# Performance work log

Hardware: AMD Instinct MI355X
Metric: run time of the kernel (lower is better)

Reference implementation:

```python
import jax, jax.numpy as jnp
import numpy as np

N = 50000      # nodes
E = 250000     # edges
IN = 256       # in_channels
OUT = 256      # out_channels
H = 4          # heads
C = OUT // H   # per-head channels = 64
MSG = 128
TIME = 64
ED = MSG + TIME + 2   # edge_dim = 194


def _glorot(k, shape):
    return (jax.random.normal(k, shape, jnp.float32) / np.sqrt(shape[0])).astype(jnp.float32)


def setup_inputs() -> dict:
    ks = jax.random.split(jax.random.key(0), 16)
    z = lambda: jnp.zeros((H * C,), jnp.float32)
    inp = {
        "x": jax.random.normal(ks[0], (N, IN), jnp.float32),
        "edge_index": jax.random.randint(ks[1], (2, E), 0, N),
        "edge_attr": jax.random.normal(ks[2], (E, ED), jnp.float32),
        # conv1 params (in_channels=IN)
        "Wq1": _glorot(ks[3], (IN, H * C)), "bq1": z(),
        "Wk1": _glorot(ks[4], (IN, H * C)), "bk1": z(),
        "Wv1": _glorot(ks[5], (IN, H * C)), "bv1": z(),
        "We1": _glorot(ks[6], (ED, H * C)),              # lin_edge has no bias in PyG
        "Ws1": _glorot(ks[7], (IN, H * C)), "bs1": z(),  # skip/root connection
        # conv2 params (in_channels=OUT)
        "Wq2": _glorot(ks[8], (OUT, H * C)), "bq2": z(),
        "Wk2": _glorot(ks[9], (OUT, H * C)), "bk2": z(),
        "Wv2": _glorot(ks[10], (OUT, H * C)), "bv2": z(),
        "We2": _glorot(ks[11], (ED, H * C)),
        "Ws2": _glorot(ks[12], (OUT, H * C)), "bs2": z(),
    }
    return inp


def _tconv(x, src, dst, edge_attr, Wq, bq, Wk, bk, Wv, bv, We, Ws, bs):
    """PyG TransformerConv (heads=H, concat=True, root_weight=True), eval mode."""
    n = x.shape[0]
    q = (x @ Wq + bq).reshape(n, H, C)
    k = (x @ Wk + bk).reshape(n, H, C)
    v = (x @ Wv + bv).reshape(n, H, C)
    e = (edge_attr @ We).reshape(-1, H, C)          # [E,H,C]
    kj = k[src] + e                                  # key + edge embedding
    vj = v[src] + e                                  # value + edge embedding
    logits = jnp.einsum('ehc,ehc->eh', q[dst], kj) / np.sqrt(C)  # [E,H]
    # segment softmax over incoming edges of each dst node
    m = jax.lax.stop_gradient(jax.ops.segment_max(logits, dst, num_segments=n))
    ex = jnp.exp(logits - m[dst])
    denom = jax.ops.segment_sum(ex, dst, num_segments=n)
    a = ex / (denom[dst] + 1e-16)                    # [E,H]
    agg = jax.ops.segment_sum(vj * a[:, :, None], dst, num_segments=n)  # [N,H,C]
    return agg.reshape(n, H * C) + x @ Ws + bs


def reference(x, edge_index, edge_attr,
              Wq1, bq1, Wk1, bk1, Wv1, bv1, We1, Ws1, bs1,
              Wq2, bq2, Wk2, bk2, Wv2, bv2, We2, Ws2, bs2):
    src, dst = edge_index[0], edge_index[1]
    h = jax.nn.relu(_tconv(x, src, dst, edge_attr,
                           Wq1, bq1, Wk1, bk1, Wv1, bv1, We1, Ws1, bs1))
    # dropout is identity in eval mode
    return _tconv(h, src, dst, edge_attr,
                  Wq2, bq2, Wk2, bk2, Wv2, bv2, We2, Ws2, bs2)
```

## Files before the change

kernel.cpp:

```cpp
#include <hip/hip_runtime.h>

#define N_NODES 50000
#define N_EDGES 250000
#define DIM 256
#define ED 194
#define EDP 224
#define MP_NODE 50048
#define MP_EDGE 250112

typedef __bf16 bf16x8 __attribute__((ext_vector_type(8)));
typedef float f32x4 __attribute__((ext_vector_type(4)));
typedef short s16x8 __attribute__((ext_vector_type(8)));
typedef short s16x4 __attribute__((ext_vector_type(4)));
typedef unsigned short u16x8 __attribute__((ext_vector_type(8)));

__device__ __forceinline__ float bf2f(unsigned short b){
  union { unsigned int u; float f; } v; v.u = ((unsigned int)b)<<16; return v.f;
}
__device__ __forceinline__ short f2bf(float f){
  union { float f; unsigned int u; } v; v.f = f;
  unsigned int u = v.u;
  return (short)((u + 0x7fffu + ((u>>16)&1u))>>16);
}

__device__ __forceinline__ void gload_lds16(const void* g, void* l){
  __builtin_amdgcn_global_load_lds(
      (const __attribute__((address_space(1))) unsigned int*)g,
      (__attribute__((address_space(3))) unsigned int*)l, 16, 0, 0);
}

__global__ __launch_bounds__(256) void convert_x_kernel(
    const float* __restrict__ x, short* __restrict__ xb, int* __restrict__ deg)
{
  int idx = blockIdx.x*256 + threadIdx.x;
  if (idx < N_NODES) deg[idx] = 0;
  s16x4 o;
  if (idx < N_NODES*64){
    float4 a = *(const float4*)(x + (size_t)idx*4);
    o[0]=f2bf(a.x); o[1]=f2bf(a.y); o[2]=f2bf(a.z); o[3]=f2bf(a.w);
  } else {
    o[0]=0; o[1]=0; o[2]=0; o[3]=0;
  }
  *(s16x4*)(xb + (size_t)idx*4) = o;
}

#define E_ROWS 32
__global__ __launch_bounds__(256) void convert_e_kernel(
    const float* __restrict__ ea, short* __restrict__ eb)
{
  __shared__ float lds[E_ROWS*ED];
  int row0 = blockIdx.x * E_ROWS;
  int tid = threadIdx.x;
  int base = row0 * ED;
  int valid = N_EDGES*ED - base;

  for (int i = tid; i < E_ROWS*ED/4; i += 256){
    float4 v;
    if (i*4 < valid) v = *(const float4*)(ea + base + i*4);
    else             v = make_float4(0.f,0.f,0.f,0.f);
    *(float4*)(lds + i*4) = v;
  }
  __syncthreads();

  for (int u = tid; u < E_ROWS*28; u += 256){
    int row = u / 28;
    int c8  = u - row*28;
    int col = c8*8;
    s16x8 o;
    if (col + 8 <= ED){
      #pragma unroll
      for (int j2=0;j2<4;j2++){
        float2 f = *(const float2*)(lds + row*ED + col + j2*2);
        o[j2*2]   = f2bf(f.x);
        o[j2*2+1] = f2bf(f.y);
      }
    } else {
      #pragma unroll
      for (int j=0;j<8;j++){
        int c = col + j;
        o[j] = (c < ED) ? f2bf(lds[row*ED + c]) : (short)0;
      }
    }
    *(s16x8*)(eb + (size_t)(row0+row)*EDP + col) = o;
  }
}

__global__ __launch_bounds__(256) void prep_weights(
    const float* __restrict__ Wq, const float* __restrict__ Wk,
    const float* __restrict__ Wv, const float* __restrict__ Ws,
    const float* __restrict__ We,
    const float* __restrict__ b0, const float* __restrict__ b1,
    const float* __restrict__ b2, const float* __restrict__ b3,
    short* __restrict__ WtN, short* __restrict__ WtE, float* __restrict__ biasN)
{
  __shared__ short lds[64*65];
  int b = blockIdx.x, tid = threadIdx.x;
  if (b < 64){
    int mat = b>>4, tile = b&15;
    int i0 = (tile>>2)*64, o0 = (tile&3)*64;
    const float* W = (mat==0)?Wq:((mat==1)?Wk:((mat==2)?Wv:Ws));
    #pragma unroll
    for (int t=0;t<16;t++){
      int idx = t*256+tid; int r = idx>>6, c = idx&63;
      lds[r*65+c] = f2bf(W[(size_t)(i0+r)*256 + o0 + c]);
    }
    __syncthreads();
    #pragma unroll
    for (int t=0;t<4;t++){
      int idx = t*256+tid; int r = idx>>4, c4 = (idx&15)*4;
      s16x4 o;
      o[0]=lds[(c4+0)*65+r]; o[1]=lds[(c4+1)*65+r];
      o[2]=lds[(c4+2)*65+r]; o[3]=lds[(c4+3)*65+r];
      *(s16x4*)(WtN + (mat<<16) + (o0+r)*256 + i0 + c4) = o;
    }
  } else if (b < 80){
    int b2 = b-64;
    int k0 = (b2>>2)*64, o0 = (b2&3)*64;
    #pragma unroll
    for (int t=0;t<16;t++){
      int idx = t*256+tid; int r = idx>>6, c = idx&63;
      int k = k0+r;
      lds[r*65+c] = (k<ED) ? f2bf(We[(size_t)k*256 + o0 + c]) : (short)0;
    }
    __syncthreads();
    #pragma unroll
    for (int t=0;t<4;t++){
      int idx = t*256+tid; int r = idx>>4, c4 = (idx&15)*4;
      if (k0 + c4 < EDP){
        s16x4 o;
        o[0]=lds[(c4+0)*65+r]; o[1]=lds[(c4+1)*65+r];
        o[2]=lds[(c4+2)*65+r]; o[3]=lds[(c4+3)*65+r];
        *(s16x4*)(WtE + (o0+r)*EDP + k0 + c4) = o;
      }
    }
  } else {
    for (int t = tid; t < 1024; t += 256){
      const float* bb = (t<256)?b0:((t<512)?b1:((t<768)?b2:b3));
      biasN[t] = bb[t&255];
    }
  }
}

__global__ __launch_bounds__(256) void count_deg(const int* __restrict__ dst, int* __restrict__ deg){
  int e = blockIdx.x*256 + threadIdx.x;
  if (e < N_EDGES) atomicAdd(&deg[dst[e]], 1);
}
#define SCAN_NBLK 196
__global__ __launch_bounds__(256) void scan_p1(const int* __restrict__ deg, int* __restrict__ part){
  int t = threadIdx.x;
  int i = blockIdx.x*256 + t;
  int v = (i<N_NODES)? deg[i] : 0;
  #pragma unroll
  for (int off=32; off; off>>=1) v += __shfl_xor(v, off, 64);
  __shared__ int s[4];
  if ((t&63)==0) s[t>>6] = v;
  __syncthreads();
  if (t==0) part[blockIdx.x] = s[0]+s[1]+s[2]+s[3];
}
__global__ __launch_bounds__(256) void scan_p2(int* __restrict__ part){
  __shared__ int s[256];
  int t = threadIdx.x;
  int v = (t<SCAN_NBLK)? part[t] : 0;
  s[t] = v; __syncthreads();
  for (int off=1; off<256; off<<=1){
    int x = (t>=off)? s[t-off] : 0;
    __syncthreads();
    s[t] += x;
    __syncthreads();
  }
  part[t] = (t==0)? 0 : s[t-1];
}
__global__ __launch_bounds__(256) void scan_p3(const int* __restrict__ deg,
    const int* __restrict__ part, int* __restrict__ rowptr, int* __restrict__ cursor){
  __shared__ int s[256];
  int t = threadIdx.x;
  int i = blockIdx.x*256 + t;
  int v = (i<N_NODES)? deg[i] : 0;
  s[t] = v; __syncthreads();
  for (int off=1; off<256; off<<=1){
    int x = (t>=off)? s[t-off] : 0;
    __syncthreads();
    s[t] += x;
    __syncthreads();
  }
  if (i < N_NODES){ rowptr[i+1] = part[blockIdx.x] + s[t]; cursor[i] = 0; }
  if (i == 0) rowptr[0] = 0;
}
__global__ __launch_bounds__(256) void scatter_edges(
    const int* __restrict__ src, const int* __restrict__ dst,
    const int* __restrict__ rowptr, int* __restrict__ cursor, int2* __restrict__ csr)
{
  int e = blockIdx.x*256 + threadIdx.x;
  if (e < N_EDGES){
    int d = dst[e];
    int pos = atomicAdd(&cursor[d], 1);
    csr[rowptr[d] + pos] = make_int2(src[e]<<11, e<<9);
  }
}

template<int K, int NLD, bool HAS_BIAS>
__global__ __launch_bounds__(256) void gemm_bt(
    const short* __restrict__ A, const short* __restrict__ Bt,
    const float* __restrict__ bias, short* __restrict__ out, int M)
{
  __shared__ short As[128*32];
  __shared__ short Bs[128*32];
  int tid = threadIdx.x;
  int lane = tid & 63, wave = tid >> 6;
  int m0 = blockIdx.x*128, n0 = blockIdx.y*128;

  int srow = wave*16 + (lane&15);
  int scol = (lane>>4)*8;
  const short* gA = A + (size_t)(m0+srow)*K + scol;
  const short* gB = Bt + (size_t)(n0+srow)*K + scol;
  short* ldsA1 = As + wave*512;
  short* ldsA2 = As + 2048 + wave*512;
  short* ldsB1 = Bs + wave*512;
  short* ldsB2 = Bs + 2048 + wave*512;

  int wr = wave>>1, wc = wave&1;
  int fr = lane & 15;
  int kq = lane >> 4;
  f32x4 acc[4][4];
  #pragma unroll
  for (int a=0;a<4;a++)
    #pragma unroll
    for (int b=0;b<4;b++) acc[a][b] = (f32x4){0.f,0.f,0.f,0.f};

  const short* ar = As + wr*2048 + kq*128 + fr*8;
  const short* br = Bs + wc*2048 + kq*128 + fr*8;

  for (int k0=0; k0<K; k0+=32){
    __syncthreads();
    gload_lds16(gA + k0,                ldsA1);
    gload_lds16(gA + (size_t)64*K + k0, ldsA2);
    gload_lds16(gB + k0,                ldsB1);
    gload_lds16(gB + (size_t)64*K + k0, ldsB2);
    __syncthreads();

    bf16x8 af[4], bf[4];
    #pragma unroll
    for (int fm=0;fm<4;fm++) af[fm] = *(const bf16x8*)(ar + fm*512);
    #pragma unroll
    for (int fn=0;fn<4;fn++) bf[fn] = *(const bf16x8*)(br + fn*512);
    #pragma unroll
    for (int fm=0;fm<4;fm++)
      #pragma unroll
      for (int fn=0;fn<4;fn++)
        acc[fm][fn] = __builtin_amdgcn_mfma_f32_16x16x32_bf16(af[fm], bf[fn], acc[fm][fn], 0, 0, 0);
  }

  int cr = (lane>>4)*4;
  int cc = lane & 15;
  #pragma unroll
  for (int fm=0;fm<4;fm++){
    #pragma unroll
    for (int fn=0;fn<4;fn++){
      int col = n0 + wc*64 + fn*16 + cc;
      float bv = HAS_BIAS ? bias[col] : 0.f;
      #pragma unroll
      for (int i=0;i<4;i++){
        int row = m0 + wr*64 + fm*16 + cr + i;
        if (row < M) out[(size_t)row*NLD + col] = f2bf(acc[fm][fn][i] + bv);
      }
    }
  }
}

__global__ __launch_bounds__(256) void edge_phase_kernel(
    const short* __restrict__ QKVS, const short* __restrict__ Eemb,
    const int* __restrict__ rowptr, const int2* __restrict__ csr,
    short* __restrict__ out_bf, float* __restrict__ out_f, int relu)
{
  int tid = threadIdx.x, wave = tid>>6, lane = tid&63;
  int node = blockIdx.x*4 + wave;
  if (node >= N_NODES){
    if (node < MP_NODE && out_bf){
      s16x4 z; z[0]=0; z[1]=0; z[2]=0; z[3]=0;
      *(s16x4*)(out_bf + (size_t)node*256 + lane*4) = z;
    }
    return;
  }
  int half = lane>>5;
  int hl   = lane&31;
  int c8   = hl*8;
  const unsigned short* base = (const unsigned short*)QKVS + (size_t)node*1024;

  u16x8 qu = *(const u16x8*)(base + c8);
  float q[8];
  #pragma unroll
  for (int j=0;j<8;j++) q[j] = bf2f(qu[j])*0.125f;

  int beg = rowptr[node], end = rowptr[node+1];
  float l = 0.f;
  float a[8];
  #pragma unroll
  for (int j=0;j<8;j++) a[j] = 0.f;
  int kb = 512 + hl*16;
  int ebo = hl*16;

  for (int idx = beg; idx < end; idx += 2){
    int j = idx + half;
    int jc = (j < end) ? j : (end-1);
    int2 se = csr[jc];
    const char* Kp = (const char*)QKVS + (unsigned)(se.x + kb);
    const char* Ep = (const char*)Eemb + (unsigned)(se.y + ebo);
    u16x8 ku = *(const u16x8*)Kp;
    u16x8 vu = *(const u16x8*)(Kp + 512);
    u16x8 eu = *(const u16x8*)Ep;
    float vv[8];
    float t = 0.f;
    #pragma unroll
    for (int c=0;c<8;c++){
      float ef = bf2f(eu[c]);
      float kf = bf2f(ku[c]) + ef;
      vv[c]    = bf2f(vu[c]) + ef;
      t += q[c]*kf;
    }
    t += __shfl_xor(t, 1, 64);
    t += __shfl_xor(t, 2, 64);
    t += __shfl_xor(t, 4, 64);
    float p = (j < end) ? __expf(t) : 0.f;
    l += p;
    #pragma unroll
    for (int c=0;c<8;c++) a[c] += p*vv[c];
  }

  l += __shfl_xor(l, 32, 64);
  #pragma unroll
  for (int c=0;c<8;c++) a[c] += __shfl_xor(a[c], 32, 64);

  float inv = (l > 0.f) ? 1.0f/l : 0.f;
  u16x8 su = *(const u16x8*)(base + 768 + c8);
  float r[8];
  #pragma unroll
  for (int c=0;c<8;c++){
    float v = a[c]*inv + bf2f(su[c]);
    r[c] = relu ? fmaxf(v, 0.f) : v;
  }

  if (out_bf){
    if (!half){
      s16x8 o;
      #pragma unroll
      for (int c=0;c<8;c++) o[c] = f2bf(r[c]);
      *(s16x8*)(out_bf + (size_t)node*256 + c8) = o;
    }
  } else {
    float4 st = half ? make_float4(r[4],r[5],r[6],r[7])
                     : make_float4(r[0],r[1],r[2],r[3]);
    *(float4*)(out_f + (size_t)node*256 + c8 + half*4) = st;
  }
}

extern "C" void kernel_launch(void* const* d_in, const int* in_sizes, int n_in,
                              void* d_out, int out_size, void* d_ws, size_t ws_size,
                              hipStream_t stream)
{
  const float* x     = (const float*)d_in[0];
  const int*   eidx  = (const int*)d_in[1];
  const float* eattr = (const float*)d_in[2];
  const float* Wq1=(const float*)d_in[3],  *bq1=(const float*)d_in[4];
  const float* Wk1=(const float*)d_in[5],  *bk1=(const float*)d_in[6];
  const float* Wv1=(const float*)d_in[7],  *bv1=(const float*)d_in[8];
  const float* We1=(const float*)d_in[9];
  const float* Ws1=(const float*)d_in[10], *bs1=(const float*)d_in[11];
  const float* Wq2=(const float*)d_in[12], *bq2=(const float*)d_in[13];
  const float* Wk2=(const float*)d_in[14], *bk2=(const float*)d_in[15];
  const float* Wv2=(const float*)d_in[16], *bv2=(const float*)d_in[17];
  const float* We2=(const float*)d_in[18];
  const float* Ws2=(const float*)d_in[19], *bs2=(const float*)d_in[20];

  char* ws = (char*)d_ws;
  size_t off = 0;
  auto alloc = [&](size_t bytes)->char*{
    char* p = ws + off; off = (off + bytes + 255) & ~(size_t)255; return p;
  };
  short* QKVS  = (short*)alloc((size_t)N_NODES*1024*2);
  short* Eemb  = (short*)alloc((size_t)N_EDGES*256*2);
  short* x_bf  = (short*)alloc((size_t)MP_NODE*DIM*2);
  short* h_bf  = (short*)alloc((size_t)MP_NODE*DIM*2);
  short* e_bf  = (short*)alloc((size_t)MP_EDGE*EDP*2);
  short* WtN   = (short*)alloc((size_t)4*65536*2);
  short* WtE   = (short*)alloc((size_t)256*EDP*2);
  float* biasN = (float*)alloc((size_t)1024*4);
  int*   deg   = (int*)alloc((size_t)N_NODES*4);
  int*   rowptr= (int*)alloc((size_t)(N_NODES+1)*4);
  int*   cursor= (int*)alloc((size_t)N_NODES*4);
  int*   part  = (int*)alloc((size_t)256*4);
  int2*  csr   = (int2*)alloc((size_t)N_EDGES*8);

  const int* srcp = eidx;
  const int* dstp = eidx + N_EDGES;

  const int EB = (N_EDGES + 255)/256;

  convert_x_kernel<<<MP_NODE*64/256,256,0,stream>>>(x, x_bf, deg);
  convert_e_kernel<<<MP_EDGE/E_ROWS,256,0,stream>>>(eattr, e_bf);

  count_deg<<<EB,256,0,stream>>>(dstp, deg);
  scan_p1<<<SCAN_NBLK,256,0,stream>>>(deg, part);
  scan_p2<<<1,256,0,stream>>>(part);
  scan_p3<<<SCAN_NBLK,256,0,stream>>>(deg, part, rowptr, cursor);
  scatter_edges<<<EB,256,0,stream>>>(srcp, dstp, rowptr, cursor, csr);

  prep_weights<<<81,256,0,stream>>>(Wq1,Wk1,Wv1,Ws1,We1,bq1,bk1,bv1,bs1,WtN,WtE,biasN);
  gemm_bt<DIM,1024,true><<<dim3(MP_NODE/128,8),256,0,stream>>>(x_bf, WtN, biasN, QKVS, N_NODES);
  gemm_bt<EDP,256,false><<<dim3(MP_EDGE/128,2),256,0,stream>>>(e_bf, WtE, nullptr, Eemb, N_EDGES);
  edge_phase_kernel<<<MP_NODE/4,256,0,stream>>>(QKVS,Eemb,rowptr,csr,h_bf,nullptr,1);

  prep_weights<<<81,256,0,stream>>>(Wq2,Wk2,Wv2,Ws2,We2,bq2,bk2,bv2,bs2,WtN,WtE,biasN);
  gemm_bt<DIM,1024,true><<<dim3(MP_NODE/128,8),256,0,stream>>>(h_bf, WtN, biasN, QKVS, N_NODES);
  gemm_bt<EDP,256,false><<<dim3(MP_EDGE/128,2),256,0,stream>>>(e_bf, WtE, nullptr, Eemb, N_EDGES);
  edge_phase_kernel<<<N_NODES/4,256,0,stream>>>(QKVS,Eemb,rowptr,csr,nullptr,(float*)d_out,0);
}
```

Baseline: 914.4 us.

## Fuse CSR build into cooperative kernel, batch weight prep, change GEMM LDS layout

Replaces the five CSR-construction kernels (degree count, three-pass scan, scatter) with one cooperative kernel that uses grid-wide syncs, and merges both layers' weight preparation into a single launch with separate buffers. This is meant to cut launch count and inter-kernel gaps. It also changes the GEMM global-to-LDS staging so each thread loads a row-contiguous 16-byte chunk, with the fragment reads adjusted to match. Grid syncs add their own latency, and the new LDS row stride of 64 bytes may cause bank conflicts on the fragment reads.

Result: slower. 1.002 ms (+9.6%).

```diff
diff --git a/kernel.cpp b/kernel.cpp
--- a/kernel.cpp
+++ b/kernel.cpp
@@ -1,4 +1,6 @@
 #include <hip/hip_runtime.h>
+#include <hip/hip_cooperative_groups.h>
+namespace cg = cooperative_groups;
 
 #define N_NODES 50000
 #define N_EDGES 250000
@@ -30,10 +32,9 @@
 }
 
 __global__ __launch_bounds__(256) void convert_x_kernel(
-    const float* __restrict__ x, short* __restrict__ xb, int* __restrict__ deg)
+    const float* __restrict__ x, short* __restrict__ xb)
 {
   int idx = blockIdx.x*256 + threadIdx.x;
-  if (idx < N_NODES) deg[idx] = 0;
   s16x4 o;
   if (idx < N_NODES*64){
     float4 a = *(const float4*)(x + (size_t)idx*4);
@@ -85,16 +86,32 @@
   }
 }
 
-__global__ __launch_bounds__(256) void prep_weights(
-    const float* __restrict__ Wq, const float* __restrict__ Wk,
-    const float* __restrict__ Wv, const float* __restrict__ Ws,
-    const float* __restrict__ We,
-    const float* __restrict__ b0, const float* __restrict__ b1,
-    const float* __restrict__ b2, const float* __restrict__ b3,
-    short* __restrict__ WtN, short* __restrict__ WtE, float* __restrict__ biasN)
+__global__ __launch_bounds__(256) void prep_weights_all(
+    const float* __restrict__ Wq1, const float* __restrict__ Wk1,
+    const float* __restrict__ Wv1, const float* __restrict__ Ws1,
+    const float* __restrict__ We1,
+    const float* __restrict__ bq1, const float* __restrict__ bk1,
+    const float* __restrict__ bv1, const float* __restrict__ bs1,
+    const float* __restrict__ Wq2, const float* __restrict__ Wk2,
+    const float* __restrict__ Wv2, const float* __restrict__ Ws2,
+    const float* __restrict__ We2,
+    const float* __restrict__ bq2, const float* __restrict__ bk2,
+    const float* __restrict__ bv2, const float* __restrict__ bs2,
+    short* __restrict__ WtN1, short* __restrict__ WtE1, float* __restrict__ biasN1,
+    short* __restrict__ WtN2, short* __restrict__ WtE2, float* __restrict__ biasN2)
 {
   __shared__ short lds[64*65];
   int b = blockIdx.x, tid = threadIdx.x;
+  const float *Wq,*Wk,*Wv,*Ws,*We,*b0,*b1,*b2,*b3;
+  short *WtN,*WtE; float* biasN;
+  if (b < 81){
+    Wq=Wq1;Wk=Wk1;Wv=Wv1;Ws=Ws1;We=We1;b0=bq1;b1=bk1;b2=bv1;b3=bs1;
+    WtN=WtN1;WtE=WtE1;biasN=biasN1;
+  } else {
+    b -= 81;
+    Wq=Wq2;Wk=Wk2;Wv=Wv2;Ws=Ws2;We=We2;b0=bq2;b1=bk2;b2=bv2;b3=bs2;
+    WtN=WtN2;WtE=WtE2;biasN=biasN2;
+  }
   if (b < 64){
     int mat = b>>4, tile = b&15;
     int i0 = (tile>>2)*64, o0 = (tile&3)*64;
@@ -141,57 +158,50 @@
   }
 }
 
-__global__ __launch_bounds__(256) void count_deg(const int* __restrict__ dst, int* __restrict__ deg){
-  int e = blockIdx.x*256 + threadIdx.x;
-  if (e < N_EDGES) atomicAdd(&deg[dst[e]], 1);
-}
-#define SCAN_NBLK 196
-__global__ __launch_bounds__(256) void scan_p1(const int* __restrict__ deg, int* __restrict__ part){
-  int t = threadIdx.x;
-  int i = blockIdx.x*256 + t;
-  int v = (i<N_NODES)? deg[i] : 0;
-  #pragma unroll
-  for (int off=32; off; off>>=1) v += __shfl_xor(v, off, 64);
-  __shared__ int s[4];
-  if ((t&63)==0) s[t>>6] = v;
-  __syncthreads();
-  if (t==0) part[blockIdx.x] = s[0]+s[1]+s[2]+s[3];
-}
-__global__ __launch_bounds__(256) void scan_p2(int* __restrict__ part){
+#define CSR_NBLK 196
+__global__ __launch_bounds__(256) void build_csr_coop(
+    const int* __restrict__ src, const int* __restrict__ dst,
+    int* __restrict__ deg, int* __restrict__ part,
+    int* __restrict__ rowptr, int* __restrict__ cursor, int2* __restrict__ csr)
+{
+  cg::grid_group grid = cg::this_grid();
   __shared__ int s[256];
-  int t = threadIdx.x;
-  int v = (t<SCAN_NBLK)? part[t] : 0;
+  int t = threadIdx.x, b = blockIdx.x;
+  int gid = b*256 + t;
+  for (int i = gid; i < N_NODES; i += CSR_NBLK*256) deg[i] = 0;
+  grid.sync();
+  for (int e = gid; e < N_EDGES; e += CSR_NBLK*256) atomicAdd(&deg[dst[e]], 1);
+  grid.sync();
+  int i = gid;
+  int v = (i < N_NODES) ? deg[i] : 0;
   s[t] = v; __syncthreads();
   for (int off=1; off<256; off<<=1){
-    int x = (t>=off)? s[t-off] : 0;
+    int x = (t>=off) ? s[t-off] : 0;
     __syncthreads();
     s[t] += x;
     __syncthreads();
   }
-  part[t] = (t==0)? 0 : s[t-1];
-}
-__global__ __launch_bounds__(256) void scan_p3(const int* __restrict__ deg,
-    const int* __restrict__ part, int* __restrict__ rowptr, int* __restrict__ cursor){
-  __shared__ int s[256];
-  int t = threadIdx.x;
-  int i = blockIdx.x*256 + t;
-  int v = (i<N_NODES)? deg[i] : 0;
-  s[t] = v; __syncthreads();
-  for (int off=1; off<256; off<<=1){
-    int x = (t>=off)? s[t-off] : 0;
-    __syncthreads();
-    s[t] += x;
-    __syncthreads();
-  }
-  if (i < N_NODES){ rowptr[i+1] = part[blockIdx.x] + s[t]; cursor[i] = 0; }
-  if (i == 0) rowptr[0] = 0;
-}
-__global__ __launch_bounds__(256) void scatter_edges(
-    const int* __restrict__ src, const int* __restrict__ dst,
-    const int* __restrict__ rowptr, int* __restrict__ cursor, int2* __restrict__ csr)
-{
-  int e = blockIdx.x*256 + threadIdx.x;
-  if (e < N_EDGES){
+  int local = s[t];
+  if (t == 255) part[b] = s[255];
+  grid.sync();
+  if (b == 0){
+    int pv = (t < CSR_NBLK) ? part[t] : 0;
+    __syncthreads();
+    s[t] = pv; __syncthreads();
+    for (int off=1; off<256; off<<=1){
+      int x = (t>=off) ? s[t-off] : 0;
+      __syncthreads();
+      s[t] += x;
+      __syncthreads();
+    }
+    part[t] = (t==0) ? 0 : s[t-1];
+  }
+  grid.sync();
+  int boff = part[b];
+  if (i < N_NODES){ rowptr[i+1] = boff + local; cursor[i] = 0; }
+  if (gid == 0) rowptr[0] = 0;
+  grid.sync();
+  for (int e = gid; e < N_EDGES; e += CSR_NBLK*256){
     int d = dst[e];
     int pos = atomicAdd(&cursor[d], 1);
     csr[rowptr[d] + pos] = make_int2(src[e]<<11, e<<9);
@@ -209,8 +219,7 @@
   int lane = tid & 63, wave = tid >> 6;
   int m0 = blockIdx.x*128, n0 = blockIdx.y*128;
 
-  int srow = wave*16 + (lane&15);
-  int scol = (lane>>4)*8;
+  int srow = tid>>2, scol = (tid&3)*8;
   const short* gA = A + (size_t)(m0+srow)*K + scol;
   const short* gB = Bt + (size_t)(n0+srow)*K + scol;
   short* ldsA1 = As + wave*512;
@@ -227,9 +236,6 @@
     #pragma unroll
     for (int b=0;b<4;b++) acc[a][b] = (f32x4){0.f,0.f,0.f,0.f};
 
-  const short* ar = As + wr*2048 + kq*128 + fr*8;
-  const short* br = Bs + wc*2048 + kq*128 + fr*8;
-
   for (int k0=0; k0<K; k0+=32){
     __syncthreads();
     gload_lds16(gA + k0,                ldsA1);
@@ -239,6 +245,8 @@
     __syncthreads();
 
     bf16x8 af[4], bf[4];
+    const short* ar = As + (wr*64 + fr)*32 + kq*8;
+    const short* br = Bs + (wc*64 + fr)*32 + kq*8;
     #pragma unroll
     for (int fm=0;fm<4;fm++) af[fm] = *(const bf16x8*)(ar + fm*512);
     #pragma unroll
@@ -381,9 +389,12 @@
   short* x_bf  = (short*)alloc((size_t)MP_NODE*DIM*2);
   short* h_bf  = (short*)alloc((size_t)MP_NODE*DIM*2);
   short* e_bf  = (short*)alloc((size_t)MP_EDGE*EDP*2);
-  short* WtN   = (short*)alloc((size_t)4*65536*2);
-  short* WtE   = (short*)alloc((size_t)256*EDP*2);
-  float* biasN = (float*)alloc((size_t)1024*4);
+  short* WtN1  = (short*)alloc((size_t)4*65536*2);
+  short* WtE1  = (short*)alloc((size_t)256*EDP*2);
+  float* biasN1= (float*)alloc((size_t)1024*4);
+  short* WtN2  = (short*)alloc((size_t)4*65536*2);
+  short* WtE2  = (short*)alloc((size_t)256*EDP*2);
+  float* biasN2= (float*)alloc((size_t)1024*4);
   int*   deg   = (int*)alloc((size_t)N_NODES*4);
   int*   rowptr= (int*)alloc((size_t)(N_NODES+1)*4);
   int*   cursor= (int*)alloc((size_t)N_NODES*4);
@@ -393,24 +404,28 @@
   const int* srcp = eidx;
   const int* dstp = eidx + N_EDGES;
 
-  const int EB = (N_EDGES + 255)/256;
-
-  convert_x_kernel<<<MP_NODE*64/256,256,0,stream>>>(x, x_bf, deg);
+  convert_x_kernel<<<MP_NODE*64/256,256,0,stream>>>(x, x_bf);
   convert_e_kernel<<<MP_EDGE/E_ROWS,256,0,stream>>>(eattr, e_bf);
 
-  count_deg<<<EB,256,0,stream>>>(dstp, deg);
-  scan_p1<<<SCAN_NBLK,256,0,stream>>>(deg, part);
-  scan_p2<<<1,256,0,stream>>>(part);
-  scan_p3<<<SCAN_NBLK,256,0,stream>>>(deg, part, rowptr, cursor);
-  scatter_edges<<<EB,256,0,stream>>>(srcp, dstp, rowptr, cursor, csr);
-
-  prep_weights<<<81,256,0,stream>>>(Wq1,Wk1,Wv1,Ws1,We1,bq1,bk1,bv1,bs1,WtN,WtE,biasN);
-  gemm_bt<DIM,1024,true><<<dim3(MP_NODE/128,8),256,0,stream>>>(x_bf, WtN, biasN, QKVS, N_NODES);
-  gemm_bt<EDP,256,false><<<dim3(MP_EDGE/128,2),256,0,stream>>>(e_bf, WtE, nullptr, Eemb, N_EDGES);
+  {
+    const int* srcp_ = srcp; const int* dstp_ = dstp;
+    int* deg_ = deg; int* part_ = part; int* rowptr_ = rowptr; int* cursor_ = cursor;
+    int2* csr_ = csr;
+    void* cargs[] = { &srcp_, &dstp_, &deg_, &part_, &rowptr_, &cursor_, &csr_ };
+    hipLaunchCooperativeKernel((void*)build_csr_coop, dim3(CSR_NBLK,1,1),
+                               dim3(256,1,1), cargs, 0, stream);
+  }
+
+  prep_weights_all<<<162,256,0,stream>>>(
+      Wq1,Wk1,Wv1,Ws1,We1,bq1,bk1,bv1,bs1,
+      Wq2,Wk2,Wv2,Ws2,We2,bq2,bk2,bv2,bs2,
+      WtN1,WtE1,biasN1, WtN2,WtE2,biasN2);
+
+  gemm_bt<DIM,1024,true><<<dim3(MP_NODE/128,8),256,0,stream>>>(x_bf, WtN1, biasN1, QKVS, N_NODES);
+  gemm_bt<EDP,256,false><<<dim3(MP_EDGE/128,2),256,0,stream>>>(e_bf, WtE1, nullptr, Eemb, N_EDGES);
   edge_phase_kernel<<<MP_NODE/4,256,0,stream>>>(QKVS,Eemb,rowptr,csr,h_bf,nullptr,1);
 
-  prep_weights<<<81,256,0,stream>>>(Wq2,Wk2,Wv2,Ws2,We2,bq2,bk2,bv2,bs2,WtN,WtE,biasN);
-  gemm_bt<DIM,1024,true><<<dim3(MP_NODE/128,8),256,0,stream>>>(h_bf, WtN, biasN, QKVS, N_NODES);
-  gemm_bt<EDP,256,false><<<dim3(MP_EDGE/128,2),256,0,stream>>>(e_bf, WtE, nullptr, Eemb, N_EDGES);
+  gemm_bt<DIM,1024,true><<<dim3(MP_NODE/128,8),256,0,stream>>>(h_bf, WtN2, biasN2, QKVS, N_NODES);
+  gemm_bt<EDP,256,false><<<dim3(MP_EDGE/128,2),256,0,stream>>>(e_bf, WtE2, nullptr, Eemb, N_EDGES);
   edge_phase_kernel<<<N_NODES/4,256,0,stream>>>(QKVS,Eemb,rowptr,csr,nullptr,(float*)d_out,0);
 }
```
